# Performance work log

Hardware: AMD Instinct MI355X
Metric: run time of the kernel (lower is better)

The kernel has to match this reference:

```python
import jax, jax.numpy as jnp
import numpy as np

KC = 32      # cluster_num
KS = 3       # kernel_size
AREA = KS * KS
ITERS = 10   # KMeans Lloyd iterations (fixed, deterministic init)


def _unfold3(x):
    # torch nn.Unfold(kernel_size=3, padding=1): feature dim ordered cin-major, area-minor
    b, c, h, w = x.shape
    xp = jnp.pad(x, ((0, 0), (0, 0), (1, 1), (1, 1)))
    cols = jnp.stack([xp[:, :, i:i + h, j:j + w] for i in range(KS) for j in range(KS)], axis=2)  # [b,c,area,h,w]
    return cols.reshape(b, c * AREA, h * w).transpose(0, 2, 1)  # [b, hw, c*area]


def _kmeans_assign(feat):
    # Lloyd's KMeans on [s, d] features; deterministic strided init; returns [s] int assignments
    s, d = feat.shape
    c0 = feat[jnp.arange(KC) * (s // KC)]
    f2 = (feat * feat).sum(-1, keepdims=True)
    def dists(c):
        return f2 - 2.0 * feat @ c.T + (c * c).sum(-1)[None, :]
    def step(c, _):
        idx = jnp.argmin(dists(c), axis=1)
        cnt = jax.ops.segment_sum(jnp.ones((s,), feat.dtype), idx, KC)
        sm = jax.ops.segment_sum(feat, idx, KC)
        c_new = jnp.where(cnt[:, None] > 0, sm / jnp.maximum(cnt, 1.0)[:, None], c)
        return c_new, None
    c, _ = jax.lax.scan(step, c0, None, length=ITERS)
    return jnp.argmin(dists(c), axis=1)


def _seg_mean(p, idx):
    # per-cluster mean of patches -> patch-space centroids [K, f]
    s = p.shape[0]
    cnt = jax.ops.segment_sum(jnp.ones((s,), p.dtype), idx, KC)
    return jax.ops.segment_sum(p, idx, KC) / jnp.maximum(cnt, 1.0)[:, None]


def _mlp2(x, W1, b1, W2, b2):
    return jax.nn.relu(jax.nn.relu(x @ W1 + b1) @ W2 + b2)


def setup_inputs():
    key = jax.random.key(0)
    ks = jax.random.split(key, 16)
    cin, cout, m = 32, 32, 16
    f = cin * AREA
    g = lambda k, shp, sc: jax.random.normal(k, shp, dtype=jnp.float32) * sc
    return {
        "x": g(ks[0], (4, cin, 64, 64), 1.0),
        "Wh1": g(ks[1], (f, m), (2.0 / f) ** 0.5), "bh1": jnp.zeros((m,), jnp.float32),
        "Wh2": g(ks[2], (m, m), (2.0 / m) ** 0.5), "bh2": jnp.zeros((m,), jnp.float32),
        "Wa": g(ks[3], (m, AREA), (2.0 / m) ** 0.5), "ba": jnp.zeros((AREA,), jnp.float32),
        "Wc": g(ks[4], (m, cin), (2.0 / m) ** 0.5), "bc": jnp.zeros((cin,), jnp.float32),
        "Wo": g(ks[5], (m, cout), (2.0 / m) ** 0.5), "bo": jnp.zeros((cout,), jnp.float32),
        "kernels": g(ks[6], (cin, AREA, cout), (2.0 / (cin * AREA)) ** 0.5),
        "Wb1": g(ks[7], (f, m), (2.0 / f) ** 0.5), "bb1": jnp.zeros((m,), jnp.float32),
        "Wb2": g(ks[8], (m, m), (2.0 / m) ** 0.5), "bb2": jnp.zeros((m,), jnp.float32),
        "Wb3": g(ks[9], (m, cout), (2.0 / m) ** 0.5), "bb3": jnp.zeros((cout,), jnp.float32),
    }


def reference(x, Wh1, bh1, Wh2, bh2, Wa, ba, Wc, bc, Wo, bo, kernels, Wb1, bb1, Wb2, bb2, Wb3, bb3):
    b, cin, h, w = x.shape
    s = h * w
    cout = kernels.shape[-1]
    patches = _unfold3(x)                                        # [b, s, cin*area]
    feat = patches.reshape(b, s, cin, AREA).mean(-1)             # cluster_source='channel'
    idx = jax.vmap(_kmeans_assign)(jax.lax.stop_gradient(feat))  # [b, s] cluster assignments
    centroids = jax.vmap(_seg_mean)(patches, idx)                # [b, K, cin*area]
    # low_rank kernel generator: rank-1 modulation along cin/area/cout of shared base kernel
    kf = _mlp2(centroids, Wh1, bh1, Wh2, bh2)                    # [b, K, m]
    w_cin = jax.nn.sigmoid(kf @ Wc + bc)                         # [b, K, cin]
    w_area = jax.nn.sigmoid(kf @ Wa + ba)                        # [b, K, area]
    w_cout = jax.nn.sigmoid(kf @ Wo + bo)                        # [b, K, cout]
    kern = (w_cin[:, :, :, None, None] * w_area[:, :, None, :, None]
            * w_cout[:, :, None, None, :] * kernels[None, None])  # [b, K, cin, area, cout]
    kern = kern.reshape(b, KC, cin * AREA, cout)
    bias = _mlp2(centroids, Wb1, bb1, Wb2, bb2) @ Wb3 + bb3      # [b, K, cout] (bias='cluster')
    # gather per-pixel kernel/bias by cluster id, grouped matmul, scatter back (dense-gather form)
    bi = jnp.arange(b)[:, None]
    Wpix = kern[bi, idx]                                         # [b, s, f, cout]
    out = jnp.einsum('bsf,bsfo->bso', patches, Wpix) + bias[bi, idx]
    return out.reshape(b, h, w, cout).transpose(0, 3, 1, 2), idx
```

## Files before the change

### kernel.cpp

```cpp
#include <hip/hip_runtime.h>
#include <stdint.h>

typedef unsigned long long u64;

#define Bn 4
#define CINn 32
#define Hn 64
#define Wn 64
#define Sn 4096
#define KCn 32
#define Mn 16
#define COUTn 32
#define AREAn 9
#define Fn 288
#define NITER 10
#define FXSCALE 4294967296.0
#define NBLK_B 16
#define PXB 256
#define CMAX 160
#define LDK 292
#define NFLAG ((NITER + 2) * Bn * NBLK_B)

#define AT_LD_U32(p)    __hip_atomic_load((p),  __ATOMIC_RELAXED, __HIP_MEMORY_SCOPE_AGENT)
#define AT_LD_U64(p)    __hip_atomic_load((p),  __ATOMIC_RELAXED, __HIP_MEMORY_SCOPE_AGENT)
#define AT_ST_U32(p,v)  __hip_atomic_store((p), (v), __ATOMIC_RELAXED, __HIP_MEMORY_SCOPE_AGENT)
#define AT_ST_U64(p,v)  __hip_atomic_store((p), (v), __ATOMIC_RELAXED, __HIP_MEMORY_SCOPE_AGENT)

static __device__ __forceinline__ float relu_(float v){ return v > 0.f ? v : 0.f; }
static __device__ __forceinline__ float sigmoid_(float v){ return 1.f / (1.f + expf(-v)); }

__global__ __launch_bounds__(256) void k_init(const float* __restrict__ x,
                                              float* __restrict__ feat,
                                              u64* __restrict__ gsum,
                                              unsigned* __restrict__ gcnt,
                                              unsigned* __restrict__ flags){
    int g = blockIdx.x * 256 + threadIdx.x;
    if (g < 3 * Bn * KCn * CINn) gsum[g] = 0ull;
    if (g < 3 * Bn * KCn)        gcnt[g] = 0u;
    if (g < NFLAG)               flags[g] = 0u;
    int p = g & (Sn - 1);
    int c = (g >> 12) & (CINn - 1);
    int b = g >> 17;
    int y = p >> 6, xx = p & 63;
    const float* xc = x + ((size_t)(b * CINn + c) << 12);
    float s = 0.f;
    #pragma unroll
    for (int i = 0; i < 3; ++i){
        int yy = y + i - 1;
        if (yy < 0 || yy >= Hn) continue;
        #pragma unroll
        for (int j = 0; j < 3; ++j){
            int xj = xx + j - 1;
            if (xj < 0 || xj >= Wn) continue;
            s += xc[(yy << 6) + xj];
        }
    }
    feat[g] = s * (1.f / 9.f);
}

struct AssignSh {
    float4 fvQ[8][PXB + 1];
    float  f2L[PXB];
    float4 cent4[KCn][8];
    float  c2[KCn];
    float  bestdM[4][PXB];
    int    bestkM[4][PXB];
    unsigned lcnt[KCn];
    unsigned off32[KCn + 1];
    unsigned scat[KCn];
    unsigned cntPrev[KCn];
    int   plist[PXB];
    int   rankF[PXB];
    unsigned baseBT[KCn];
};
struct SmkSh {
    float psum[CINn][AREAn][8];
    float centL[Fn];
    int   pl[256];
    float part1[16][16], part2[16][16];
    float hL[2][Mn];
    float kfL[2][Mn];
};
union ShU { AssignSh a; SmkSh m; };

__global__ __launch_bounds__(256) void k_main(const float* __restrict__ x,
        const float* __restrict__ feat,
        u64* __restrict__ gsum, unsigned* __restrict__ gcnt,
        unsigned* __restrict__ blkcnt,
        float* __restrict__ idxf,
        int* __restrict__ sorted, int4* __restrict__ chunk_map,
        const float* __restrict__ Wh1, const float* __restrict__ bh1,
        const float* __restrict__ Wh2, const float* __restrict__ bh2,
        const float* __restrict__ Wa,  const float* __restrict__ ba,
        const float* __restrict__ Wc,  const float* __restrict__ bc,
        const float* __restrict__ Wo,  const float* __restrict__ bo,
        const float* __restrict__ Wb1, const float* __restrict__ bb1,
        const float* __restrict__ Wb2, const float* __restrict__ bb2,
        const float* __restrict__ Wb3, const float* __restrict__ bb3,
        float* __restrict__ wcin, float* __restrict__ warea,
        float* __restrict__ wcout, float* __restrict__ biasb,
        unsigned* __restrict__ flg){
    __shared__ int bi256[PXB];
    __shared__ unsigned totK[KCn];
    __shared__ unsigned goffK[KCn + 1];
    __shared__ unsigned chunkOff[KCn + 1];
    __shared__ ShU sh;

    const int tid  = threadIdx.x;
    const int b    = blockIdx.x >> 4;
    const int tnum = blockIdx.x & 15;
    const int p    = tnum * PXB + tid;
    const int kq   = tid >> 6;
    const int pxb  = tid & 63;

    float fv[CINn];
    #pragma unroll
    for (int cq = 0; cq < 8; ++cq){
        float4 v;
        v.x = feat[(b * CINn + cq * 4 + 0) * Sn + p];
        v.y = feat[(b * CINn + cq * 4 + 1) * Sn + p];
        v.z = feat[(b * CINn + cq * 4 + 2) * Sn + p];
        v.w = feat[(b * CINn + cq * 4 + 3) * Sn + p];
        sh.a.fvQ[cq][tid] = v;
        fv[cq * 4 + 0] = v.x; fv[cq * 4 + 1] = v.y;
        fv[cq * 4 + 2] = v.z; fv[cq * 4 + 3] = v.w;
    }
    {
        float s = 0.f;
        #pragma unroll
        for (int c = 0; c < CINn; ++c) s = fmaf(fv[c], fv[c], s);
        sh.a.f2L[tid] = s;
    }
    __syncthreads();

    for (int iter = 0; iter <= NITER; ++iter){
        const int prev = (iter + 2) % 3;
        const int cur  = iter % 3;
        const int nxt  = (iter + 1) % 3;

        if (iter == 0){
            float* centf = (float*)sh.a.cent4;
            for (int e = tid; e < KCn * CINn; e += 256){
                int k = e >> 5, c = e & 31;
                centf[e] = feat[(b * CINn + c) * Sn + k * (Sn / KCn)];
            }
        } else {
            if (tid < NBLK_B)
                while (AT_LD_U32(&flg[(iter - 1) * Bn * NBLK_B + b * NBLK_B + tid]) == 0u)
                    __builtin_amdgcn_s_sleep(2);
            __syncthreads();
            if (tid < KCn)
                sh.a.cntPrev[tid] = AT_LD_U32(&gcnt[(prev * Bn + b) * KCn + tid]);
            u64 sv[4];
            #pragma unroll
            for (int q = 0; q < 4; ++q)
                sv[q] = AT_LD_U64(&gsum[(size_t)(prev * Bn + b) * 1024 + tid + q * 256]);
            __syncthreads();
            float* centf = (float*)sh.a.cent4;
            #pragma unroll
            for (int q = 0; q < 4; ++q){
                const int e = tid + q * 256;
                unsigned cn = sh.a.cntPrev[e >> 5];
                if (cn > 0)
                    centf[e] = (float)((double)(long long)sv[q] / ((double)cn * FXSCALE));
            }
        }
        if (iter < NITER && tnum == 0){
            for (int e = tid; e < KCn * CINn; e += 256)
                AT_ST_U64(&gsum[(size_t)(nxt * Bn + b) * 1024 + e], 0ull);
            if (tid < KCn) AT_ST_U32(&gcnt[(nxt * Bn + b) * KCn + tid], 0u);
        }
        __syncthreads();
        if (tid < KCn){
            const float4* cr = sh.a.cent4[tid];
            float s = 0.f;
            #pragma unroll
            for (int cq2 = 0; cq2 < 8; ++cq2){
                float4 v = cr[cq2];
                s = fmaf(v.x, v.x, s); s = fmaf(v.y, v.y, s);
                s = fmaf(v.z, v.z, s); s = fmaf(v.w, v.w, s);
            }
            sh.a.c2[tid] = s;
            sh.a.lcnt[tid] = 0u;
            sh.a.scat[tid] = 0u;
        }
        __syncthreads();

        float dot[4][8];
        #pragma unroll
        for (int j = 0; j < 4; ++j)
            #pragma unroll
            for (int kk = 0; kk < 8; ++kk) dot[j][kk] = 0.f;
        #pragma unroll
        for (int cq2 = 0; cq2 < 8; ++cq2){
            float4 fr0 = sh.a.fvQ[cq2][pxb];
            float4 fr1 = sh.a.fvQ[cq2][pxb + 64];
            float4 fr2 = sh.a.fvQ[cq2][pxb + 128];
            float4 fr3 = sh.a.fvQ[cq2][pxb + 192];
            #pragma unroll
            for (int kk = 0; kk < 8; ++kk){
                float4 cv = sh.a.cent4[kq * 8 + kk][cq2];
                dot[0][kk] = fmaf(fr0.x, cv.x, dot[0][kk]); dot[0][kk] = fmaf(fr0.y, cv.y, dot[0][kk]);
                dot[0][kk] = fmaf(fr0.z, cv.z, dot[0][kk]); dot[0][kk] = fmaf(fr0.w, cv.w, dot[0][kk]);
                dot[1][kk] = fmaf(fr1.x, cv.x, dot[1][kk]); dot[1][kk] = fmaf(fr1.y, cv.y, dot[1][kk]);
                dot[1][kk] = fmaf(fr1.z, cv.z, dot[1][kk]); dot[1][kk] = fmaf(fr1.w, cv.w, dot[1][kk]);
                dot[2][kk] = fmaf(fr2.x, cv.x, dot[2][kk]); dot[2][kk] = fmaf(fr2.y, cv.y, dot[2][kk]);
                dot[2][kk] = fmaf(fr2.z, cv.z, dot[2][kk]); dot[2][kk] = fmaf(fr2.w, cv.w, dot[2][kk]);
                dot[3][kk] = fmaf(fr3.x, cv.x, dot[3][kk]); dot[3][kk] = fmaf(fr3.y, cv.y, dot[3][kk]);
                dot[3][kk] = fmaf(fr3.z, cv.z, dot[3][kk]); dot[3][kk] = fmaf(fr3.w, cv.w, dot[3][kk]);
            }
        }
        #pragma unroll
        for (int j = 0; j < 4; ++j){
            const int px = pxb + 64 * j;
            const float f2v = sh.a.f2L[px];
            float bd = 3.402823466e38f; int bkk = kq * 8;
            #pragma unroll
            for (int kk = 0; kk < 8; ++kk){
                float d = f2v - 2.f * dot[j][kk] + sh.a.c2[kq * 8 + kk];
                if (d < bd){ bd = d; bkk = kq * 8 + kk; }
            }
            sh.a.bestdM[kq][px] = bd;
            sh.a.bestkM[kq][px] = bkk;
        }
        __syncthreads();
        int bk;
        {
            float bd = sh.a.bestdM[0][tid]; bk = sh.a.bestkM[0][tid];
            #pragma unroll
            for (int q = 1; q < 4; ++q){
                float d2 = sh.a.bestdM[q][tid];
                if (d2 < bd){ bd = d2; bk = sh.a.bestkM[q][tid]; }
            }
            bi256[tid] = bk;
        }

        if (iter < NITER){
            atomicAdd(&sh.a.lcnt[bk], 1u);
            __syncthreads();
            if (tid == 0){
                unsigned acc = 0;
                #pragma unroll
                for (int k = 0; k < KCn; ++k){ sh.a.off32[k] = acc; acc += sh.a.lcnt[k]; }
                sh.a.off32[KCn] = acc;
            }
            __syncthreads();
            {
                unsigned pos = sh.a.off32[bk] + atomicAdd(&sh.a.scat[bk], 1u);
                sh.a.plist[pos] = tid;
            }
            __syncthreads();
            {
                const int wv   = tid >> 6;
                const int lane = tid & 63;
                const int hf   = lane >> 5;
                const int c    = lane & 31;
                const float* fvf = (const float*)sh.a.fvQ;
                #pragma unroll
                for (int kq2 = 0; kq2 < 8; ++kq2){
                    const int k  = wv * 8 + kq2;
                    const int o0 = (int)sh.a.off32[k];
                    const int n  = (int)sh.a.off32[k + 1] - o0;
                    u64 acc = 0ull;
                    for (int i = hf; i < n; i += 2){
                        int px = sh.a.plist[o0 + i];
                        float fvv = fvf[(c >> 2) * 1028 + px * 4 + (c & 3)];
                        acc += (u64)llrint((double)fvv * FXSCALE);
                    }
                    acc += __shfl_down(acc, 32);
                    if (lane < 32 && n > 0)
                        atomicAdd(&gsum[(size_t)(cur * Bn + b) * 1024 + k * 32 + c], acc);
                }
            }
            if (tid < KCn){
                unsigned v = sh.a.lcnt[tid];
                if (v) atomicAdd(&gcnt[(cur * Bn + b) * KCn + tid], v);
            }
            __syncthreads();
            if (tid == 0)
                AT_ST_U32(&flg[iter * Bn * NBLK_B + b * NBLK_B + tnum], 1u);
        } else {
            idxf[b * Sn + p] = (float)bk;
            __syncthreads();
            if (tid < KCn){
                int r = 0;
                for (int q = 0; q < PXB; ++q)
                    if (bi256[q] == tid) sh.a.rankF[q] = r++;
                AT_ST_U32(&blkcnt[(b * KCn + tid) * NBLK_B + tnum], (unsigned)r);
            }
            __syncthreads();
            if (tid == 0)
                AT_ST_U32(&flg[NITER * Bn * NBLK_B + b * NBLK_B + tnum], 1u);
        }
    }

    if (tid < NBLK_B)
        while (AT_LD_U32(&flg[NITER * Bn * NBLK_B + b * NBLK_B + tid]) == 0u)
            __builtin_amdgcn_s_sleep(2);
    __syncthreads();
    if (tid < KCn){
        unsigned run = 0, mybase = 0;
        #pragma unroll 4
        for (int blk = 0; blk < NBLK_B; ++blk){
            unsigned v = AT_LD_U32(&blkcnt[(b * KCn + tid) * NBLK_B + blk]);
            if (blk == tnum) mybase = run;
            run += v;
        }
        totK[tid] = run;
        sh.a.baseBT[tid] = mybase;
    }
    __syncthreads();
    if (tid == 0){
        unsigned acc = 0;
        #pragma unroll
        for (int k = 0; k < KCn; ++k){ goffK[k] = acc; acc += totK[k]; }
        goffK[KCn] = acc;
    }
    __syncthreads();
    {
        int k = bi256[tid];
        unsigned pos = goffK[k] + sh.a.baseBT[k] + (unsigned)sh.a.rankF[tid];
        AT_ST_U32((unsigned*)&sorted[b * Sn + pos], (unsigned)p);
    }
    if (tnum == 0){
        if (tid == 0){
            unsigned acc = 0;
            #pragma unroll
            for (int k = 0; k < KCn; ++k){ chunkOff[k] = acc; acc += (totK[k] + 31) >> 5; }
            chunkOff[KCn] = acc;
        }
        __syncthreads();
        if (tid < KCn){
            int n = (int)totK[tid];
            unsigned j0 = chunkOff[tid];
            for (int cb = 0; cb < n; cb += 32)
                chunk_map[b * CMAX + (j0++)] = make_int4(tid, (int)goffK[tid] + cb, min(32, n - cb), 0);
        }
        for (int j = (int)chunkOff[KCn] + tid; j < CMAX; j += 256)
            chunk_map[b * CMAX + j] = make_int4(-1, 0, 0, 0);
    }
    __syncthreads();
    if (tid == 0)
        AT_ST_U32(&flg[(NITER + 1) * Bn * NBLK_B + b * NBLK_B + tnum], 1u);
    if (tid < NBLK_B)
        while (AT_LD_U32(&flg[(NITER + 1) * Bn * NBLK_B + b * NBLK_B + tid]) == 0u)
            __builtin_amdgcn_s_sleep(2);
    __syncthreads();

    for (int kq2 = 0; kq2 < 2; ++kq2){
        const int kk   = tnum * 2 + kq2;
        const int off0 = (int)goffK[kk];
        const int nmy  = (int)totK[kk];
        __syncthreads();
        {
            const int cA = tid >> 3;
            const int s  = tid & 7;
            const float* xc = x + ((size_t)(b * CINn + cA) << 12);
            float acc[9];
            #pragma unroll
            for (int a = 0; a < 9; ++a) acc[a] = 0.f;
            for (int base = 0; base < nmy; base += 256){
                int m = min(256, nmy - base);
                __syncthreads();
                if (tid < m)
                    sh.m.pl[tid] = (int)AT_LD_U32((unsigned*)&sorted[b * Sn + off0 + base + tid]);
                __syncthreads();
                #pragma unroll 2
                for (int i = s; i < m; i += 8){
                    int pp = sh.m.pl[i];
                    int py = pp >> 6, px2 = pp & 63;
                    #pragma unroll
                    for (int a = 0; a < 9; ++a){
                        int y1 = py + a / 3 - 1, x1 = px2 + (a % 3) - 1;
                        float v = (y1 >= 0 && y1 < Hn && x1 >= 0 && x1 < Wn)
                                  ? xc[(y1 << 6) + x1] : 0.f;
                        acc[a] += v;
                    }
                }
            }
            __syncthreads();
            #pragma unroll
            for (int a = 0; a < 9; ++a) sh.m.psum[cA][a][s] = acc[a];
            __syncthreads();
            float invn = 1.f / (float)max(nmy, 1);
            for (int f = tid; f < Fn; f += 256){
                int c = f / 9, a = f - c * 9;
                float sm = 0.f;
                #pragma unroll
                for (int s2 = 0; s2 < 8; ++s2) sm += sh.m.psum[c][a][s2];
                sh.m.centL[f] = sm * invn;
            }
        }
        __syncthreads();
        {
            int j = tid & 15, rep = tid >> 4;
            float p1 = 0.f, p2 = 0.f;
            int fbeg = rep * 18;
            for (int ff = fbeg; ff < fbeg + 18; ++ff){
                float cv = sh.m.centL[ff];
                p1 = fmaf(cv, Wh1[ff * Mn + j], p1);
                p2 = fmaf(cv, Wb1[ff * Mn + j], p2);
            }
            sh.m.part1[rep][j] = p1;
            sh.m.part2[rep][j] = p2;
        }
        __syncthreads();
        if (tid < 32){
            int br = tid >> 4, j = tid & 15;
            float s = br ? bb1[j] : bh1[j];
            for (int r = 0; r < 16; ++r) s += br ? sh.m.part2[r][j] : sh.m.part1[r][j];
            sh.m.hL[br][j] = relu_(s);
        }
        __syncthreads();
        if (tid < 32){
            int br = tid >> 4, j = tid & 15;
            const float* W2 = br ? Wb2 : Wh2;
            float s = br ? bb2[j] : bh2[j];
            #pragma unroll
            for (int i = 0; i < Mn; ++i) s = fmaf(sh.m.hL[br][i], W2[i * Mn + j], s);
            sh.m.kfL[br][j] = relu_(s);
        }
        __syncthreads();
        if (tid < 32){
            int o = tid;
            float s1 = bc[o], s2 = bo[o], s3 = bb3[o];
            #pragma unroll
            for (int i = 0; i < Mn; ++i){
                float kv = sh.m.kfL[0][i];
                s1 = fmaf(kv, Wc[i * COUTn + o], s1);
                s2 = fmaf(kv, Wo[i * COUTn + o], s2);
                s3 = fmaf(sh.m.kfL[1][i], Wb3[i * COUTn + o], s3);
            }
            wcin [(b * KCn + kk) * CINn  + o] = sigmoid_(s1);
            wcout[(b * KCn + kk) * COUTn + o] = sigmoid_(s2);
            biasb[(b * KCn + kk) * COUTn + o] = s3;
        } else if (tid < 41){
            int a2 = tid - 32;
            float s = ba[a2];
            #pragma unroll
            for (int i = 0; i < Mn; ++i) s = fmaf(sh.m.kfL[0][i], Wa[i * AREAn + a2], s);
            warea[(b * KCn + kk) * AREAn + a2] = sigmoid_(s);
        }
    }
}

__global__ __launch_bounds__(256) void k_out(const float* __restrict__ x,
                                             const int* __restrict__ sorted,
                                             const int4* __restrict__ chunk_map,
                                             const float* __restrict__ wcin,
                                             const float* __restrict__ warea,
                                             const float* __restrict__ wcout,
                                             const float* __restrict__ biasb,
                                             const float* __restrict__ kern0,
                                             float* __restrict__ out){
    const int b   = blockIdx.x / CMAX;
    const int j   = blockIdx.x - b * CMAX;
    const int tid = threadIdx.x;

    int4 cm = chunk_map[b * CMAX + j];
    const int kcur = cm.x;
    if (kcur < 0) return;
    const int base = cm.y;
    const int cnt  = cm.z;

    __shared__ float kernT[COUTn * LDK];
    __shared__ float patchL[32 * LDK];
    __shared__ int   pix[32];
    __shared__ float wcl[CINn], wal[AREAn], wol[COUTn], biasL[COUTn];

    if (tid < 32){
        pix[tid] = (tid < cnt) ? sorted[b * Sn + base + tid] : -1;
    } else if (tid < 64)  wcl[tid - 32]    = wcin [(b * KCn + kcur) * CINn  + tid - 32];
    else if (tid < 96)    wol[tid - 64]    = wcout[(b * KCn + kcur) * COUTn + tid - 64];
    else if (tid < 105)   wal[tid - 96]    = warea[(b * KCn + kcur) * AREAn + tid - 96];
    else if (tid >= 128 && tid < 160) biasL[tid - 128] = biasb[(b * KCn + kcur) * COUTn + tid - 128];

    const int fA = tid;       const int cA = fA / 9, aA = fA - cA * 9;
    const int dyA = aA / 3 - 1, dxA = aA % 3 - 1;
    const int fB = 256 + tid; const int cB = fB / 9, aB = fB - cB * 9;
    const int dyB = aB / 3 - 1, dxB = aB % 3 - 1;
    __syncthreads();

    {
        int o  = tid >> 3;
        int q  = tid & 7;
        int f0 = q * 36;
        int cc = q * 4, aa = 0;
        float wo_ = wol[o];
        float* kr = kernT + o * LDK + f0;
        #pragma unroll 4
        for (int i2 = 0; i2 < 36; ++i2){
            kr[i2] = wcl[cc] * wal[aa] * wo_ * kern0[(f0 + i2) * COUTn + o];
            if (++aa == 9){ aa = 0; ++cc; }
        }
    }

    #pragma unroll 4
    for (int px = 0; px < 32; ++px){
        int pp = pix[px];
        float vA = 0.f, vB = 0.f;
        if (pp >= 0){
            int py = pp >> 6, pxx = pp & 63;
            int y1 = py + dyA, x1 = pxx + dxA;
            if (y1 >= 0 && y1 < Hn && x1 >= 0 && x1 < Wn)
                vA = x[((size_t)(b * CINn + cA) << 12) + (y1 << 6) + x1];
            if (tid < 32){
                int y2 = py + dyB, x2 = pxx + dxB;
                if (y2 >= 0 && y2 < Hn && x2 >= 0 && x2 < Wn)
                    vB = x[((size_t)(b * CINn + cB) << 12) + (y2 << 6) + x2];
            }
        }
        patchL[px * LDK + tid] = vA;
        if (tid < 32) patchL[px * LDK + 256 + tid] = vB;
    }
    __syncthreads();

    const int o2 = tid & 15, p2 = tid >> 4;
    const int oA = o2, oB = o2 + 16;
    const int pxA = p2, pxB = p2 + 16;
    const bool actA = pxA < cnt, actB = pxB < cnt;
    if (!actA && !actB) return;

    const float* krA = kernT + oA * LDK;
    const float* krB = kernT + oB * LDK;
    const float* prA = patchL + pxA * LDK;
    const float* prB = patchL + pxB * LDK;
    float s00 = 0.f, s01 = 0.f, s10 = 0.f, s11 = 0.f;
    #pragma unroll 4
    for (int fq = 0; fq < Fn; fq += 4){
        float4 k0 = *reinterpret_cast<const float4*>(krA + fq);
        float4 k1 = *reinterpret_cast<const float4*>(krB + fq);
        float4 pa = *reinterpret_cast<const float4*>(prA + fq);
        float4 pb = *reinterpret_cast<const float4*>(prB + fq);
        s00 = fmaf(pa.x,k0.x,s00); s00 = fmaf(pa.y,k0.y,s00); s00 = fmaf(pa.z,k0.z,s00); s00 = fmaf(pa.w,k0.w,s00);
        s01 = fmaf(pa.x,k1.x,s01); s01 = fmaf(pa.y,k1.y,s01); s01 = fmaf(pa.z,k1.z,s01); s01 = fmaf(pa.w,k1.w,s01);
        s10 = fmaf(pb.x,k0.x,s10); s10 = fmaf(pb.y,k0.y,s10); s10 = fmaf(pb.z,k0.z,s10); s10 = fmaf(pb.w,k0.w,s10);
        s11 = fmaf(pb.x,k1.x,s11); s11 = fmaf(pb.y,k1.y,s11); s11 = fmaf(pb.z,k1.z,s11); s11 = fmaf(pb.w,k1.w,s11);
    }
    if (actA){
        int pp = pix[pxA];
        out[((size_t)(b * COUTn + oA) << 12) + pp] = biasL[oA] + s00;
        out[((size_t)(b * COUTn + oB) << 12) + pp] = biasL[oB] + s01;
    }
    if (actB){
        int pp = pix[pxB];
        out[((size_t)(b * COUTn + oA) << 12) + pp] = biasL[oA] + s10;
        out[((size_t)(b * COUTn + oB) << 12) + pp] = biasL[oB] + s11;
    }
}

extern "C" void kernel_launch(void* const* d_in, const int* in_sizes, int n_in,
                              void* d_out, int out_size, void* d_ws, size_t ws_size,
                              hipStream_t stream){
    const float* x    = (const float*)d_in[0];
    const float* Wh1  = (const float*)d_in[1];
    const float* bh1  = (const float*)d_in[2];
    const float* Wh2  = (const float*)d_in[3];
    const float* bh2  = (const float*)d_in[4];
    const float* Wa   = (const float*)d_in[5];
    const float* ba   = (const float*)d_in[6];
    const float* Wc   = (const float*)d_in[7];
    const float* bc   = (const float*)d_in[8];
    const float* Wo   = (const float*)d_in[9];
    const float* bo   = (const float*)d_in[10];
    const float* kern0= (const float*)d_in[11];
    const float* Wb1  = (const float*)d_in[12];
    const float* bb1  = (const float*)d_in[13];
    const float* Wb2  = (const float*)d_in[14];
    const float* bb2  = (const float*)d_in[15];
    const float* Wb3  = (const float*)d_in[16];
    const float* bb3  = (const float*)d_in[17];

    char* ws = (char*)d_ws;
    float*    feat    = (float*)(ws + 0);
    u64*      gsum    = (u64*)  (ws + 2097152);
    unsigned* gcnt    = (unsigned*)(ws + 2195456);
    unsigned* blkcnt  = (unsigned*)(ws + 2196992);
    int*      sorted  = (int*)  (ws + 2205184);
    float*    wcin    = (float*)(ws + 2270720);
    float*    warea   = (float*)(ws + 2287104);
    float*    wcout   = (float*)(ws + 2291712);
    float*    biasb   = (float*)(ws + 2308096);
    int4*     chunk_map = (int4*)(ws + 2324480);
    unsigned* flags   = (unsigned*)(ws + 2334720);

    float* outp = (float*)d_out;
    float* idxf = outp + (size_t)Bn * COUTn * Sn;

    k_init<<<(Bn * CINn * Sn) / 256, 256, 0, stream>>>(x, feat, gsum, gcnt, flags);
    k_main<<<Bn * NBLK_B, 256, 0, stream>>>(x, feat, gsum, gcnt, blkcnt, idxf,
                                            sorted, chunk_map,
                                            Wh1, bh1, Wh2, bh2, Wa, ba, Wc, bc, Wo, bo,
                                            Wb1, bb1, Wb2, bb2, Wb3, bb3,
                                            wcin, warea, wcout, biasb, flags);
    k_out<<<Bn * CMAX, 256, 0, stream>>>(x, sorted, chunk_map, wcin, warea, wcout,
                                         biasb, kern0, outp);
}
```

Baseline: 217.8 us.

## Balance patch-centroid accumulation across blocks via sorted-range runs and atomics

Previously each block computed patch-space centroid sums for two fixed clusters, so the work per block followed cluster sizes and could be very uneven. Now each block takes an equal 256-entry slice of the cluster-sorted pixel list, which carries the cluster id packed into the high bits. It splits the slice into runs by cluster and atomically adds partial sums into a global buffer, then waits on an extra grid-wide flag barrier before the MLP stage. The per-iteration clearing of the next sums buffer also moves across blocks instead of always block 0. This costs float atomics, a serial run scan in thread 0, an additional inter-block barrier, and an accumulation order that is no longer deterministic.

```diff
diff --git a/kernel.cpp b/kernel.cpp
--- a/kernel.cpp
+++ b/kernel.cpp
@@ -19,7 +19,7 @@
 #define PXB 256
 #define CMAX 160
 #define LDK 292
-#define NFLAG ((NITER + 2) * Bn * NBLK_B)
+#define NFLAG ((NITER + 3) * Bn * NBLK_B)
 
 #define AT_LD_U32(p)    __hip_atomic_load((p),  __ATOMIC_RELAXED, __HIP_MEMORY_SCOPE_AGENT)
 #define AT_LD_U64(p)    __hip_atomic_load((p),  __ATOMIC_RELAXED, __HIP_MEMORY_SCOPE_AGENT)
@@ -33,10 +33,12 @@
                                               float* __restrict__ feat,
                                               u64* __restrict__ gsum,
                                               unsigned* __restrict__ gcnt,
+                                              float* __restrict__ gpsum,
                                               unsigned* __restrict__ flags){
     int g = blockIdx.x * 256 + threadIdx.x;
     if (g < 3 * Bn * KCn * CINn) gsum[g] = 0ull;
     if (g < 3 * Bn * KCn)        gcnt[g] = 0u;
+    if (g < Bn * KCn * Fn)       gpsum[g] = 0.f;
     if (g < NFLAG)               flags[g] = 0u;
     int p = g & (Sn - 1);
     int c = (g >> 12) & (CINn - 1);
@@ -76,7 +78,9 @@
 struct SmkSh {
     float psum[CINn][AREAn][8];
     float centL[Fn];
-    int   pl[256];
+    int   spl[PXB];
+    int   runK[33], runS[33], runE[33];
+    int   nruns;
     float part1[16][16], part2[16][16];
     float hL[2][Mn];
     float kfL[2][Mn];
@@ -99,6 +103,7 @@
         const float* __restrict__ Wb3, const float* __restrict__ bb3,
         float* __restrict__ wcin, float* __restrict__ warea,
         float* __restrict__ wcout, float* __restrict__ biasb,
+        float* __restrict__ gpsum,
         unsigned* __restrict__ flg){
     __shared__ int bi256[PXB];
     __shared__ unsigned totK[KCn];
@@ -151,7 +156,7 @@
             __syncthreads();
             if (tid < KCn)
                 sh.a.cntPrev[tid] = AT_LD_U32(&gcnt[(prev * Bn + b) * KCn + tid]);
-            u64 sv[4];
+        u64 sv[4];
             #pragma unroll
             for (int q = 0; q < 4; ++q)
                 sv[q] = AT_LD_U64(&gsum[(size_t)(prev * Bn + b) * 1024 + tid + q * 256]);
@@ -165,7 +170,7 @@
                     centf[e] = (float)((double)(long long)sv[q] / ((double)cn * FXSCALE));
             }
         }
-        if (iter < NITER && tnum == 0){
+        if (iter < NITER && tnum == (iter & 15)){
             for (int e = tid; e < KCn * CINn; e += 256)
                 AT_ST_U64(&gsum[(size_t)(nxt * Bn + b) * 1024 + e], 0ull);
             if (tid < KCn) AT_ST_U32(&gcnt[(nxt * Bn + b) * KCn + tid], 0u);
@@ -320,7 +325,7 @@
     {
         int k = bi256[tid];
         unsigned pos = goffK[k] + sh.a.baseBT[k] + (unsigned)sh.a.rankF[tid];
-        AT_ST_U32((unsigned*)&sorted[b * Sn + pos], (unsigned)p);
+        AT_ST_U32((unsigned*)&sorted[b * Sn + pos], (unsigned)(p | (k << 16)));
     }
     if (tnum == 0){
         if (tid == 0){
@@ -347,50 +352,79 @@
             __builtin_amdgcn_s_sleep(2);
     __syncthreads();
 
-    for (int kq2 = 0; kq2 < 2; ++kq2){
-        const int kk   = tnum * 2 + kq2;
-        const int off0 = (int)goffK[kk];
-        const int nmy  = (int)totK[kk];
-        __syncthreads();
-        {
-            const int cA = tid >> 3;
-            const int s  = tid & 7;
-            const float* xc = x + ((size_t)(b * CINn + cA) << 12);
+    {
+        sh.m.spl[tid] = (int)AT_LD_U32((unsigned*)&sorted[b * Sn + tnum * PXB + tid]);
+        __syncthreads();
+        if (tid == 0){
+            int nr = 0, s0 = 0, kcur = sh.m.spl[0] >> 16;
+            for (int i = 1; i < PXB; ++i){
+                int kx = sh.m.spl[i] >> 16;
+                if (kx != kcur){
+                    sh.m.runK[nr] = kcur; sh.m.runS[nr] = s0; sh.m.runE[nr] = i;
+                    ++nr; kcur = kx; s0 = i;
+                }
+            }
+            sh.m.runK[nr] = kcur; sh.m.runS[nr] = s0; sh.m.runE[nr] = PXB;
+            sh.m.nruns = nr + 1;
+        }
+        __syncthreads();
+        const int cc = tid >> 3;
+        const int sl = tid & 7;
+        const float* xc = x + ((size_t)(b * CINn + cc) << 12);
+        const int nruns = sh.m.nruns;
+        for (int r = 0; r < nruns; ++r){
+            const int ks = sh.m.runK[r];
+            const int i0 = sh.m.runS[r], i1 = sh.m.runE[r];
             float acc[9];
             #pragma unroll
             for (int a = 0; a < 9; ++a) acc[a] = 0.f;
-            for (int base = 0; base < nmy; base += 256){
-                int m = min(256, nmy - base);
-                __syncthreads();
-                if (tid < m)
-                    sh.m.pl[tid] = (int)AT_LD_U32((unsigned*)&sorted[b * Sn + off0 + base + tid]);
-                __syncthreads();
-                #pragma unroll 2
-                for (int i = s; i < m; i += 8){
-                    int pp = sh.m.pl[i];
-                    int py = pp >> 6, px2 = pp & 63;
-                    #pragma unroll
-                    for (int a = 0; a < 9; ++a){
-                        int y1 = py + a / 3 - 1, x1 = px2 + (a % 3) - 1;
-                        float v = (y1 >= 0 && y1 < Hn && x1 >= 0 && x1 < Wn)
-                                  ? xc[(y1 << 6) + x1] : 0.f;
-                        acc[a] += v;
-                    }
+            for (int i = i0 + sl; i < i1; i += 8){
+                int pp = sh.m.spl[i] & 0xFFFF;
+                int py = pp >> 6, px2 = pp & 63;
+                #pragma unroll
+                for (int a = 0; a < 9; ++a){
+                    int y1 = py + a / 3 - 1, x1 = px2 + (a % 3) - 1;
+                    float v = (y1 >= 0 && y1 < Hn && x1 >= 0 && x1 < Wn)
+                              ? xc[(y1 << 6) + x1] : 0.f;
+                    acc[a] += v;
                 }
             }
-            __syncthreads();
-            #pragma unroll
-            for (int a = 0; a < 9; ++a) sh.m.psum[cA][a][s] = acc[a];
-            __syncthreads();
-            float invn = 1.f / (float)max(nmy, 1);
-            for (int f = tid; f < Fn; f += 256){
+            #pragma unroll
+            for (int a = 0; a < 9; ++a) sh.m.psum[cc][a][sl] = acc[a];
+            __syncthreads();
+            {
+                int f = tid;
                 int c = f / 9, a = f - c * 9;
                 float sm = 0.f;
                 #pragma unroll
                 for (int s2 = 0; s2 < 8; ++s2) sm += sh.m.psum[c][a][s2];
-                sh.m.centL[f] = sm * invn;
-            }
-        }
+                atomicAdd(&gpsum[((size_t)b * KCn + ks) * Fn + f], sm);
+                if (tid < 32){
+                    int f2i = 256 + tid;
+                    int c2i = f2i / 9, a2i = f2i - c2i * 9;
+                    float sm2 = 0.f;
+                    #pragma unroll
+                    for (int s2 = 0; s2 < 8; ++s2) sm2 += sh.m.psum[c2i][a2i][s2];
+                    atomicAdd(&gpsum[((size_t)b * KCn + ks) * Fn + f2i], sm2);
+                }
+            }
+            __syncthreads();
+        }
+    }
+    __syncthreads();
+    if (tid == 0)
+        AT_ST_U32(&flg[(NITER + 2) * Bn * NBLK_B + b * NBLK_B + tnum], 1u);
+    if (tid < NBLK_B)
+        while (AT_LD_U32(&flg[(NITER + 2) * Bn * NBLK_B + b * NBLK_B + tid]) == 0u)
+            __builtin_amdgcn_s_sleep(2);
+    __syncthreads();
+
+    for (int kq2 = 0; kq2 < 2; ++kq2){
+        const int kk = tnum * 2 + kq2;
+        const float invn = 1.f / (float)max(totK[kk], 1u);
+        __syncthreads();
+        for (int f = tid; f < Fn; f += 256)
+            sh.m.centL[f] = __uint_as_float(AT_LD_U32((unsigned*)&gpsum[((size_t)b * KCn + kk) * Fn + f])) * invn;
         __syncthreads();
         {
             int j = tid & 15, rep = tid >> 4;
@@ -469,7 +503,7 @@
     __shared__ float wcl[CINn], wal[AREAn], wol[COUTn], biasL[COUTn];
 
     if (tid < 32){
-        pix[tid] = (tid < cnt) ? sorted[b * Sn + base + tid] : -1;
+        pix[tid] = (tid < cnt) ? (sorted[b * Sn + base + tid] & 0xFFFF) : -1;
     } else if (tid < 64)  wcl[tid - 32]    = wcin [(b * KCn + kcur) * CINn  + tid - 32];
     else if (tid < 96)    wol[tid - 64]    = wcout[(b * KCn + kcur) * COUTn + tid - 64];
     else if (tid < 105)   wal[tid - 96]    = warea[(b * KCn + kcur) * AREAn + tid - 96];
@@ -577,22 +611,23 @@
     unsigned* gcnt    = (unsigned*)(ws + 2195456);
     unsigned* blkcnt  = (unsigned*)(ws + 2196992);
     int*      sorted  = (int*)  (ws + 2205184);
-    float*    wcin    = (float*)(ws + 2270720);
-    float*    warea   = (float*)(ws + 2287104);
-    float*    wcout   = (float*)(ws + 2291712);
-    float*    biasb   = (float*)(ws + 2308096);
-    int4*     chunk_map = (int4*)(ws + 2324480);
-    unsigned* flags   = (unsigned*)(ws + 2334720);
+    float*    gpsum   = (float*)(ws + 2270720);
+    float*    wcin    = (float*)(ws + 2418176);
+    float*    warea   = (float*)(ws + 2434560);
+    float*    wcout   = (float*)(ws + 2439168);
+    float*    biasb   = (float*)(ws + 2455552);
+    int4*     chunk_map = (int4*)(ws + 2471936);
+    unsigned* flags   = (unsigned*)(ws + 2482176);
 
     float* outp = (float*)d_out;
     float* idxf = outp + (size_t)Bn * COUTn * Sn;
 
-    k_init<<<(Bn * CINn * Sn) / 256, 256, 0, stream>>>(x, feat, gsum, gcnt, flags);
+    k_init<<<(Bn * CINn * Sn) / 256, 256, 0, stream>>>(x, feat, gsum, gcnt, gpsum, flags);
     k_main<<<Bn * NBLK_B, 256, 0, stream>>>(x, feat, gsum, gcnt, blkcnt, idxf,
                                             sorted, chunk_map,
                                             Wh1, bh1, Wh2, bh2, Wa, ba, Wc, bc, Wo, bo,
                                             Wb1, bb1, Wb2, bb2, Wb3, bb3,
-                                            wcin, warea, wcout, biasb, flags);
+                                            wcin, warea, wcout, biasb, gpsum, flags);
     k_out<<<Bn * CMAX, 256, 0, stream>>>(x, sorted, chunk_map, wcin, warea, wcout,
                                          biasb, kern0, outp);
 }
```

Result: slower. 227.9 us (+4.6%).
